# Kernel optimization log

Measured on AMD Instinct MI355X. Metric: run time of the kernel, lower is better.

The kernel has to match this reference:

```python
import jax, jax.numpy as jnp
import numpy as np

V, B, E, T = 100000, 4096, 128, 2
H = 4 * E  # GNN hidden size = 512


def setup_inputs() -> dict:
    key = jax.random.key(0)
    ks = jax.random.split(key, 24)
    stdv = 1.0 / np.sqrt(H)
    u = lambda k, shp: jax.random.uniform(k, shp, jnp.float32, -stdv, stdv)
    return {
        "A": jax.random.uniform(ks[0], (B, 13, 13), jnp.float32),
        "input_ids": jax.random.randint(ks[1], (B, 52), 0, V),
        "emb": jax.random.normal(ks[2], (V, E), jnp.float32) * 0.02,
        "b_ah": u(ks[3], (H,)),
        "w_z": u(ks[4], (H, H)), "b_wz": u(ks[5], (H,)),
        "u_z": u(ks[6], (H, H)), "b_uz": u(ks[7], (H,)),
        "w_r": u(ks[8], (H, H)), "b_wr": u(ks[9], (H,)),
        "u_r": u(ks[10], (H, H)), "b_ur": u(ks[11], (H,)),
        "w": u(ks[12], (H, H)), "b_w": u(ks[13], (H,)),
        "u_": u(ks[14], (H, H)), "b_u": u(ks[15], (H,)),
        "w1": u(ks[16], (H // 2, H)), "b1": u(ks[17], (H // 2,)),
        "w12": u(ks[18], (1, H // 2)), "b12": u(ks[19], (1,)),
        "w2": u(ks[20], (H // 2, H)), "b2": u(ks[21], (H // 2,)),
        "w22": u(ks[22], (1, H // 2)), "b22": u(ks[23], (1,)),
    }


def _sgnn_forward(A, input_ids, emb,
                  b_ah, w_z, b_wz, u_z, b_uz, w_r, b_wr, u_r, b_ur,
                  w, b_w, u_, b_u,
                  w1, b1, w12, b12, w2, b2, w22, b22):
    hid = emb[input_ids]                                        # [B,52,E]
    # cat the 4 fields of each of the 13 nodes -> [B,13,4E]
    h = jnp.concatenate([hid[:, i * 13:(i + 1) * 13, :] for i in range(4)], axis=2)
    At = jnp.swapaxes(A, 1, 2)                                  # [B,13,13]
    for _ in range(T):  # GGNN recurrence, GRU-style cell
        a = jnp.matmul(At, h) + b_ah                            # [B,13,H]
        z = jax.nn.sigmoid(a @ w_z.T + b_wz + h @ u_z.T + b_uz)
        r = jax.nn.sigmoid(a @ w_r.T + b_wr + h @ u_r.T + b_ur)
        c = jnp.tanh(a @ w.T + b_w + (r * h) @ u_.T + b_u)
        h = (1.0 - z) * h + z * c
    gnn_out = h                                                 # [B,13,H]
    ctx = gnn_out[:, 0:8, :]                                    # [B,8,H]
    # repeat(1,5,1).view(5B,8,H): 5 copies of each sample's context
    input_a = jnp.repeat(ctx[:, None, :, :], 5, axis=1).reshape(5 * B, 8, H)
    input_b = gnn_out[:, 8:13, :].reshape(5 * B, H)             # candidates
    # attention over the 8 context events per candidate
    u_a2 = jax.nn.relu(jax.nn.relu(input_a @ w1.T + b1) @ w12.T + b12)  # [5B,8,1]
    u_b2 = jax.nn.relu(jax.nn.relu(input_b @ w2.T + b2) @ w22.T + b22)  # [5B,1]
    u_c = u_a2.reshape(5 * B, 8) + u_b2.reshape(5 * B, 1)
    weight = jnp.exp(jnp.tanh(u_c))
    weight = (weight / jnp.sum(weight, axis=1, keepdims=True))[..., None]
    a_vec = jnp.sum(input_a * weight, axis=1)                   # [5B,H]
    scores = -jnp.sqrt(jnp.sum((a_vec - input_b) ** 2, axis=1))  # euclid metric
    return scores.reshape(B, 5)


def reference(A, input_ids, emb,
              b_ah, w_z, b_wz, u_z, b_uz, w_r, b_wr, u_r, b_ur,
              w, b_w, u_, b_u,
              w1, b1, w12, b12, w2, b2, w22, b22):
    return _sgnn_forward(A, input_ids, emb,
                         b_ah, w_z, b_wz, u_z, b_uz, w_r, b_wr, u_r, b_ur,
                         w, b_w, u_, b_u,
                         w1, b1, w12, b12, w2, b2, w22, b22)
```

## Files before the change

### kernel.cpp

```cpp
#include <hip/hip_runtime.h>
#include <hip/hip_bf16.h>
#include <math.h>

#define HDIM 512

typedef __attribute__((ext_vector_type(8))) __bf16 bf16x8;
typedef __attribute__((ext_vector_type(2))) __bf16 bf16x2;
typedef __attribute__((ext_vector_type(4))) float f32x4;

#define GLOAD16(src, dst) __builtin_amdgcn_global_load_lds( \
    (const __attribute__((address_space(1))) void*)(src),   \
    (__attribute__((address_space(3))) void*)(dst), 16, 0, 0)

__device__ __forceinline__ float sigmoidf_(float x) { return 1.0f / (1.0f + __expf(-x)); }

__global__ __launch_bounds__(256) void f2bf_all(
    const float* __restrict__ w_z, const float* __restrict__ u_z,
    const float* __restrict__ w_r, const float* __restrict__ u_r,
    const float* __restrict__ w_, const float* __restrict__ u_u,
    const float* __restrict__ w1, const float* __restrict__ w2,
    __bf16* __restrict__ Wzb, __bf16* __restrict__ Uzb,
    __bf16* __restrict__ Wrb, __bf16* __restrict__ Urb,
    __bf16* __restrict__ Wb, __bf16* __restrict__ Ub,
    __bf16* __restrict__ W1b, __bf16* __restrict__ W2b) {
    int bid = blockIdx.x;
    const float* s; __bf16* d; int base;
    if (bid < 1024)      { s = w_z; d = Wzb; base = bid; }
    else if (bid < 2048) { s = u_z; d = Uzb; base = bid - 1024; }
    else if (bid < 3072) { s = w_r; d = Wrb; base = bid - 2048; }
    else if (bid < 4096) { s = u_r; d = Urb; base = bid - 3072; }
    else if (bid < 5120) { s = w_;  d = Wb;  base = bid - 4096; }
    else if (bid < 6144) { s = u_u; d = Ub;  base = bid - 5120; }
    else if (bid < 6656) { s = w1;  d = W1b; base = bid - 6144; }
    else                 { s = w2;  d = W2b; base = bid - 6656; }
    int i = base * 256 + threadIdx.x;
    d[i] = (__bf16)s[i];
}

__global__ __launch_bounds__(256) void gather_a(
    const int* __restrict__ ids, const float* __restrict__ emb,
    const float* __restrict__ Ain, const float* __restrict__ bah,
    __bf16* __restrict__ Hbf, __bf16* __restrict__ Abf) {
    int b = blockIdx.x;
    int c2 = threadIdx.x;
    __shared__ float As[169];
    __shared__ int sid[52];
    if (c2 < 169) As[c2] = Ain[b * 169 + c2];
    if (c2 < 52) sid[c2] = ids[b * 52 + c2];
    __syncthreads();
    int c0 = c2 * 2;
    int iseg = c0 >> 7, e = c0 & 127;
    float h0[13], h1[13];
#pragma unroll
    for (int j = 0; j < 13; ++j) {
        int id = sid[iseg * 13 + j];
        float2 hv = *(const float2*)&emb[(size_t)id * 128 + e];
        h0[j] = hv.x;
        h1[j] = hv.y;
        bf16x2 o;
        o[0] = (__bf16)hv.x;
        o[1] = (__bf16)hv.y;
        *(bf16x2*)&Hbf[(size_t)(b * 13 + j) * HDIM + c0] = o;
    }
    float bb0 = bah[c0], bb1 = bah[c0 + 1];
#pragma unroll
    for (int i = 0; i < 13; ++i) {
        float a0 = bb0, a1 = bb1;
#pragma unroll
        for (int j = 0; j < 13; ++j) {
            float a = As[j * 13 + i];
            a0 = fmaf(a, h0[j], a0);
            a1 = fmaf(a, h1[j], a1);
        }
        bf16x2 o;
        o[0] = (__bf16)a0;
        o[1] = (__bf16)a1;
        *(bf16x2*)&Abf[(size_t)(b * 13 + i) * HDIM + c0] = o;
    }
}

__global__ __launch_bounds__(256) void a_kernel(const float* __restrict__ Ain,
                                                const __bf16* __restrict__ Hbf,
                                                const float* __restrict__ bah,
                                                __bf16* __restrict__ Abf) {
    int b = blockIdx.x;
    int c2 = threadIdx.x;
    __shared__ float As[169];
    if (c2 < 169) As[c2] = Ain[b * 169 + c2];
    float h0[13], h1[13];
#pragma unroll
    for (int j = 0; j < 13; ++j) {
        bf16x2 hv = *(const bf16x2*)&Hbf[(size_t)(b * 13 + j) * HDIM + c2 * 2];
        h0[j] = (float)hv[0];
        h1[j] = (float)hv[1];
    }
    __syncthreads();
    float bb0 = bah[c2 * 2], bb1 = bah[c2 * 2 + 1];
#pragma unroll
    for (int i = 0; i < 13; ++i) {
        float acc0 = bb0, acc1 = bb1;
#pragma unroll
        for (int j = 0; j < 13; ++j) {
            float a = As[j * 13 + i];
            acc0 = fmaf(a, h0[j], acc0);
            acc1 = fmaf(a, h1[j], acc1);
        }
        bf16x2 o;
        o[0] = (__bf16)acc0;
        o[1] = (__bf16)acc1;
        *(bf16x2*)&Abf[(size_t)(b * 13 + i) * HDIM + c2 * 2] = o;
    }
}

__global__ __launch_bounds__(512) void zr_fused(
    const __bf16* __restrict__ Abf, const __bf16* __restrict__ Hbf,
    const __bf16* __restrict__ Wz, const __bf16* __restrict__ Uz,
    const __bf16* __restrict__ Wr, const __bf16* __restrict__ Ur,
    const float* __restrict__ bwz, const float* __restrict__ buz,
    const float* __restrict__ bwr, const float* __restrict__ bur,
    __bf16* __restrict__ Zbf, __bf16* __restrict__ RHbf) {
    __shared__ __bf16 lA[2][4096];
    __shared__ __bf16 lB[2][8192];
    int t = threadIdx.x;
    int w = t >> 6, lane = t & 63;
    int role = w & 1;
    int wq = w >> 1;
    int wr2 = wq >> 1, wc2 = wq & 1;
    int m_base = blockIdx.x * 128;
    int n_base = blockIdx.y * 128;

    f32x4 acc[4][4];
#pragma unroll
    for (int i = 0; i < 4; ++i)
#pragma unroll
        for (int j = 0; j < 4; ++j)
#pragma unroll
            for (int q = 0; q < 4; ++q) acc[i][j][q] = 0.0f;

    int srow = t >> 2;
    int scol = ((t & 3) ^ ((t >> 3) & 3)) << 3;
    size_t aoff = (size_t)(m_base + srow) * HDIM + scol;
    size_t boff = (size_t)(n_base + srow) * HDIM + scol;
    int frow = lane & 15, kg = lane >> 4;
    int rsl = kg ^ ((frow >> 1) & 3);

    auto stage = [&](int step, int buf) {
        int seg = step >> 4;
        int kc = (step & 15) << 5;
        const __bf16* Xp = seg ? Hbf : Abf;
        const __bf16* B0 = seg ? Uz : Wz;
        const __bf16* B1 = seg ? Ur : Wr;
        GLOAD16(Xp + aoff + kc, &lA[buf][w * 512]);
        GLOAD16(B0 + boff + kc, &lB[buf][w * 512]);
        GLOAD16(B1 + boff + kc, &lB[buf][4096 + w * 512]);
    };

    stage(0, 0);
    int cur = 0;
    for (int step = 0; step < 32; ++step) {
        if (step < 31) {
            stage(step + 1, cur ^ 1);
            asm volatile("s_waitcnt vmcnt(3)" ::: "memory");
        } else {
            asm volatile("s_waitcnt vmcnt(0)" ::: "memory");
        }
        __builtin_amdgcn_s_barrier();
        bf16x8 af[4], bfr[4];
#pragma unroll
        for (int i = 0; i < 4; ++i) {
            af[i] = *(const bf16x8*)&lA[cur][(wr2 * 64 + i * 16 + frow) * 32 + rsl * 8];
            bfr[i] = *(const bf16x8*)&lB[cur][role * 4096 + (wc2 * 64 + i * 16 + frow) * 32 + rsl * 8];
        }
        __builtin_amdgcn_s_setprio(1);
#pragma unroll
        for (int i = 0; i < 4; ++i)
#pragma unroll
            for (int j = 0; j < 4; ++j)
                acc[i][j] = __builtin_amdgcn_mfma_f32_16x16x32_bf16(af[i], bfr[j], acc[i][j], 0, 0, 0);
        __builtin_amdgcn_s_setprio(0);
        __builtin_amdgcn_s_barrier();
        cur ^= 1;
    }

    int frow4 = (lane >> 4) * 4;
    int fcol = lane & 15;
#pragma unroll
    for (int i = 0; i < 4; ++i) {
#pragma unroll
        for (int j = 0; j < 4; ++j) {
            int col = n_base + wc2 * 64 + j * 16 + fcol;
            float bias = role ? (bwr[col] + bur[col]) : (bwz[col] + buz[col]);
            int rbase = m_base + wr2 * 64 + i * 16 + frow4;
#pragma unroll
            for (int q = 0; q < 4; ++q) {
                size_t off = (size_t)(rbase + q) * HDIM + col;
                float v = sigmoidf_(acc[i][j][q] + bias);
                if (role) {
                    RHbf[off] = (__bf16)(v * (float)Hbf[off]);
                } else {
                    Zbf[off] = (__bf16)v;
                }
            }
        }
    }
}

__global__ __launch_bounds__(512) void c_fused(
    const __bf16* __restrict__ Abf, const __bf16* __restrict__ RHbf,
    const __bf16* __restrict__ W, const __bf16* __restrict__ U,
    const float* __restrict__ bw, const float* __restrict__ bu,
    const __bf16* __restrict__ Zbf, float* __restrict__ Hf, __bf16* __restrict__ Hbf,
    int lastIter) {
    __shared__ __bf16 lA[2][4096];
    __shared__ __bf16 lB[2][4096];
    int t = threadIdx.x;
    int w = t >> 6, lane = t & 63;
    int wr = w >> 2, wc = w & 3;
    int m_base = blockIdx.x * 128;
    int n_base = blockIdx.y * 128;

    f32x4 acc[4][2];
#pragma unroll
    for (int i = 0; i < 4; ++i)
#pragma unroll
        for (int j = 0; j < 2; ++j)
#pragma unroll
            for (int q = 0; q < 4; ++q) acc[i][j][q] = 0.0f;

    int srow = t >> 2;
    int scol = ((t & 3) ^ ((t >> 3) & 3)) << 3;
    size_t aoff = (size_t)(m_base + srow) * HDIM + scol;
    size_t boff = (size_t)(n_base + srow) * HDIM + scol;
    int frow = lane & 15, kg = lane >> 4;
    int rsl = kg ^ ((frow >> 1) & 3);

    auto stage = [&](int step, int buf) {
        int seg = step >> 4;
        int kc = (step & 15) << 5;
        const __bf16* Xp = seg ? RHbf : Abf;
        const __bf16* Wp = seg ? U : W;
        GLOAD16(Xp + aoff + kc, &lA[buf][w * 512]);
        GLOAD16(Wp + boff + kc, &lB[buf][w * 512]);
    };

    stage(0, 0);
    int cur = 0;
    for (int step = 0; step < 32; ++step) {
        if (step < 31) {
            stage(step + 1, cur ^ 1);
            asm volatile("s_waitcnt vmcnt(2)" ::: "memory");
        } else {
            asm volatile("s_waitcnt vmcnt(0)" ::: "memory");
        }
        __builtin_amdgcn_s_barrier();
        bf16x8 af[4], bfr[2];
#pragma unroll
        for (int i = 0; i < 4; ++i)
            af[i] = *(const bf16x8*)&lA[cur][(wr * 64 + i * 16 + frow) * 32 + rsl * 8];
#pragma unroll
        for (int j = 0; j < 2; ++j)
            bfr[j] = *(const bf16x8*)&lB[cur][(wc * 32 + j * 16 + frow) * 32 + rsl * 8];
        __builtin_amdgcn_s_setprio(1);
#pragma unroll
        for (int i = 0; i < 4; ++i)
#pragma unroll
            for (int j = 0; j < 2; ++j)
                acc[i][j] = __builtin_amdgcn_mfma_f32_16x16x32_bf16(af[i], bfr[j], acc[i][j], 0, 0, 0);
        __builtin_amdgcn_s_setprio(0);
        __builtin_amdgcn_s_barrier();
        cur ^= 1;
    }

    int frow4 = (lane >> 4) * 4;
    int fcol = lane & 15;
#pragma unroll
    for (int i = 0; i < 4; ++i) {
#pragma unroll
        for (int j = 0; j < 2; ++j) {
            int col = n_base + wc * 32 + j * 16 + fcol;
            float bias = bw[col] + bu[col];
            int rbase = m_base + wr * 64 + i * 16 + frow4;
#pragma unroll
            for (int q = 0; q < 4; ++q) {
                size_t off = (size_t)(rbase + q) * HDIM + col;
                float v = acc[i][j][q] + bias;
                float x = v > 15.0f ? 15.0f : (v < -15.0f ? -15.0f : v);
                float e = __expf(2.0f * x);
                float cv = (e - 1.0f) / (e + 1.0f);
                float h = (float)Hbf[off];
                float z = (float)Zbf[off];
                float hn = (1.0f - z) * h + z * cv;
                Hbf[off] = (__bf16)hn;
                if (lastIter) Hf[off] = hn;
            }
        }
    }
}

__global__ __launch_bounds__(512) void score_mfma(
    const __bf16* __restrict__ Hbf,
    const __bf16* __restrict__ W1b, const __bf16* __restrict__ W2b,
    const float* __restrict__ b1A, const float* __restrict__ b1B,
    const float* __restrict__ wsA, const float* __restrict__ wsB,
    const float* __restrict__ b2A, const float* __restrict__ b2B,
    float* __restrict__ UA, float* __restrict__ UB, int nblkA) {
    __shared__ __bf16 lA[2][4096];
    __shared__ __bf16 lB[2][8192];
    __shared__ float red[128][5];
    int t = threadIdx.x;
    int w = t >> 6, lane = t & 63;
    int wr = w >> 2, wc = w & 3;

    const __bf16* Wb;
    const float* bias1;
    const float* wsm;
    const float* bias2;
    float* outv;
    int inner, off, m_base;
    if ((int)blockIdx.x < nblkA) {
        Wb = W1b; bias1 = b1A; wsm = wsA; bias2 = b2A; outv = UA;
        inner = 8; off = 0; m_base = blockIdx.x * 128;
    } else {
        Wb = W2b; bias1 = b1B; wsm = wsB; bias2 = b2B; outv = UB;
        inner = 5; off = 8; m_base = (blockIdx.x - nblkA) * 128;
    }

    f32x4 acc[4][4];
#pragma unroll
    for (int i = 0; i < 4; ++i)
#pragma unroll
        for (int j = 0; j < 4; ++j)
#pragma unroll
            for (int q = 0; q < 4; ++q) acc[i][j][q] = 0.0f;

    int srow = t >> 2;
    int scol = ((t & 3) ^ ((t >> 3) & 3)) << 3;
    int mrow = m_base + srow;
    int hrow = (mrow / inner) * 13 + off + (mrow % inner);
    size_t aoff = (size_t)hrow * HDIM + scol;
    size_t boff = (size_t)srow * HDIM + scol;
    int frow = lane & 15, kg = lane >> 4;
    int rsl = kg ^ ((frow >> 1) & 3);

    auto stage = [&](int step, int buf) {
        int kc = step << 5;
        GLOAD16(Hbf + aoff + kc, &lA[buf][w * 512]);
        GLOAD16(Wb + boff + kc, &lB[buf][w * 512]);
        GLOAD16(Wb + boff + (size_t)128 * HDIM + kc, &lB[buf][4096 + w * 512]);
    };

    stage(0, 0);
    int cur = 0;
    for (int step = 0; step < 16; ++step) {
        if (step < 15) {
            stage(step + 1, cur ^ 1);
            asm volatile("s_waitcnt vmcnt(3)" ::: "memory");
        } else {
            asm volatile("s_waitcnt vmcnt(0)" ::: "memory");
        }
        __builtin_amdgcn_s_barrier();
        bf16x8 af[4], bfr[4];
#pragma unroll
        for (int i = 0; i < 4; ++i) {
            af[i] = *(const bf16x8*)&lA[cur][(wr * 64 + i * 16 + frow) * 32 + rsl * 8];
            bfr[i] = *(const bf16x8*)&lB[cur][(wc * 64 + i * 16 + frow) * 32 + rsl * 8];
        }
        __builtin_amdgcn_s_setprio(1);
#pragma unroll
        for (int i = 0; i < 4; ++i)
#pragma unroll
            for (int j = 0; j < 4; ++j)
                acc[i][j] = __builtin_amdgcn_mfma_f32_16x16x32_bf16(af[i], bfr[j], acc[i][j], 0, 0, 0);
        __builtin_amdgcn_s_setprio(0);
        __builtin_amdgcn_s_barrier();
        cur ^= 1;
    }

    int frow4 = (lane >> 4) * 4;
    int fcol = lane & 15;
#pragma unroll
    for (int i = 0; i < 4; ++i) {
#pragma unroll
        for (int q = 0; q < 4; ++q) {
            float s = 0.0f;
#pragma unroll
            for (int j = 0; j < 4; ++j) {
                int col = wc * 64 + j * 16 + fcol;
                float v = acc[i][j][q] + bias1[col];
                v = v > 0.0f ? v : 0.0f;
                s = fmaf(v, wsm[col], s);
            }
            s += __shfl_xor(s, 1);
            s += __shfl_xor(s, 2);
            s += __shfl_xor(s, 4);
            s += __shfl_xor(s, 8);
            if (fcol == 0) red[wr * 64 + i * 16 + frow4 + q][wc] = s;
        }
    }
    __syncthreads();
    if (t < 128) {
        float s = red[t][0] + red[t][1] + red[t][2] + red[t][3] + bias2[0];
        outv[m_base + t] = s > 0.0f ? s : 0.0f;
    }
}

__global__ __launch_bounds__(256) void final_kernel(const float* __restrict__ H,
                                                    const float* __restrict__ UAv,
                                                    const float* __restrict__ UBv,
                                                    float* __restrict__ outv) {
    int b = blockIdx.x;
    int t = threadIdx.x;
    __shared__ float ctx[8][512];
    __shared__ float uas[8], ubs[5];
    __shared__ float red[4];
#pragma unroll
    for (int q = 0; q < 16; ++q) {
        int idx = q * 256 + t;
        int j = idx >> 9, c = idx & 511;
        ctx[j][c] = H[(size_t)(b * 13 + j) * HDIM + c];
    }
    if (t < 8) uas[t] = UAv[b * 8 + t];
    if (t < 5) ubs[t] = UBv[b * 5 + t];
    __syncthreads();
    int c0 = t, c1 = t + 256;
    int wid = t >> 6, lane = t & 63;
    for (int s = 0; s < 5; ++s) {
        float wn[8];
        float sum = 0.0f;
#pragma unroll
        for (int j = 0; j < 8; ++j) {
            wn[j] = __expf(tanhf(uas[j] + ubs[s]));
            sum += wn[j];
        }
        float inv = 1.0f / sum;
        float av0 = 0.0f, av1 = 0.0f;
#pragma unroll
        for (int j = 0; j < 8; ++j) {
            av0 = fmaf(wn[j], ctx[j][c0], av0);
            av1 = fmaf(wn[j], ctx[j][c1], av1);
        }
        av0 *= inv;
        av1 *= inv;
        float d0 = av0 - H[(size_t)(b * 13 + 8 + s) * HDIM + c0];
        float d1 = av1 - H[(size_t)(b * 13 + 8 + s) * HDIM + c1];
        float v = d0 * d0 + d1 * d1;
#pragma unroll
        for (int o = 32; o > 0; o >>= 1) v += __shfl_down(v, o);
        if (lane == 0) red[wid] = v;
        __syncthreads();
        if (t == 0) outv[b * 5 + s] = -sqrtf(red[0] + red[1] + red[2] + red[3]);
        __syncthreads();
    }
}

extern "C" void kernel_launch(void* const* d_in, const int* in_sizes, int n_in,
                              void* d_out, int out_size, void* d_ws, size_t ws_size,
                              hipStream_t stream) {
    const float* Ain  = (const float*)d_in[0];
    const int*   ids  = (const int*)d_in[1];
    const float* emb  = (const float*)d_in[2];
    const float* b_ah = (const float*)d_in[3];
    const float* w_z  = (const float*)d_in[4];
    const float* b_wz = (const float*)d_in[5];
    const float* u_z  = (const float*)d_in[6];
    const float* b_uz = (const float*)d_in[7];
    const float* w_r  = (const float*)d_in[8];
    const float* b_wr = (const float*)d_in[9];
    const float* u_r  = (const float*)d_in[10];
    const float* b_ur = (const float*)d_in[11];
    const float* w_   = (const float*)d_in[12];
    const float* b_w  = (const float*)d_in[13];
    const float* u_u  = (const float*)d_in[14];
    const float* b_u  = (const float*)d_in[15];
    const float* w1   = (const float*)d_in[16];
    const float* b1   = (const float*)d_in[17];
    const float* w12  = (const float*)d_in[18];
    const float* b12  = (const float*)d_in[19];
    const float* w2   = (const float*)d_in[20];
    const float* b2   = (const float*)d_in[21];
    const float* w22  = (const float*)d_in[22];
    const float* b22  = (const float*)d_in[23];
    float* out = (float*)d_out;

    int C = 128;
    {
        const int cands[6] = {4096, 2048, 1024, 512, 256, 128};
        for (int ci = 0; ci < 6; ++ci) {
            int cc = cands[ci];
            size_t rows = (size_t)13 * cc;
            size_t need = rows * 512 * 12
                        + 6 * (size_t)262144 * 2
                        + 2 * (size_t)131072 * 2
                        + (size_t)13 * cc * 4
                        + (4u << 20);
            if (need <= ws_size) { C = cc; break; }
        }
    }
    const int rows = 13 * C;

    char* base = (char*)d_ws;
    __bf16* Wzb = (__bf16*)base; base += 262144 * 2;
    __bf16* Uzb = (__bf16*)base; base += 262144 * 2;
    __bf16* Wrb = (__bf16*)base; base += 262144 * 2;
    __bf16* Urb = (__bf16*)base; base += 262144 * 2;
    __bf16* Wb  = (__bf16*)base; base += 262144 * 2;
    __bf16* Ub  = (__bf16*)base; base += 262144 * 2;
    __bf16* W1b = (__bf16*)base; base += 131072 * 2;
    __bf16* W2b = (__bf16*)base; base += 131072 * 2;
    float* UA  = (float*)base; base += (size_t)8 * C * 4;
    float* UB  = (float*)base; base += (size_t)5 * C * 4;
    float* Hf  = (float*)base; base += (size_t)rows * 512 * 4;
    __bf16* Hbf  = (__bf16*)base; base += (size_t)rows * 512 * 2;
    __bf16* Abf  = (__bf16*)base; base += (size_t)rows * 512 * 2;
    __bf16* RHbf = (__bf16*)base; base += (size_t)rows * 512 * 2;
    __bf16* Zbf  = (__bf16*)base; base += (size_t)rows * 512 * 2;

    f2bf_all<<<7168, 256, 0, stream>>>(w_z, u_z, w_r, u_r, w_, u_u, w1, w2,
                                       Wzb, Uzb, Wrb, Urb, Wb, Ub, W1b, W2b);

    dim3 ggrid(rows / 128, 4);
    int nblkA = 8 * C / 128;
    int nblkB = 5 * C / 128;
    for (int g0 = 0; g0 < 4096; g0 += C) {
        gather_a<<<C, 256, 0, stream>>>(ids + (size_t)g0 * 52, emb,
                                        Ain + (size_t)g0 * 169, b_ah, Hbf, Abf);
        zr_fused<<<ggrid, 512, 0, stream>>>(Abf, Hbf, Wzb, Uzb, Wrb, Urb,
                                            b_wz, b_uz, b_wr, b_ur, Zbf, RHbf);
        c_fused<<<ggrid, 512, 0, stream>>>(Abf, RHbf, Wb, Ub, b_w, b_u, Zbf, Hf, Hbf, 0);
        a_kernel<<<C, 256, 0, stream>>>(Ain + (size_t)g0 * 169, Hbf, b_ah, Abf);
        zr_fused<<<ggrid, 512, 0, stream>>>(Abf, Hbf, Wzb, Uzb, Wrb, Urb,
                                            b_wz, b_uz, b_wr, b_ur, Zbf, RHbf);
        c_fused<<<ggrid, 512, 0, stream>>>(Abf, RHbf, Wb, Ub, b_w, b_u, Zbf, Hf, Hbf, 1);

        score_mfma<<<nblkA + nblkB, 512, 0, stream>>>(Hbf, W1b, W2b, b1, b2, w12, w22,
                                                      b12, b22, UA, UB, nblkA);
        final_kernel<<<C, 256, 0, stream>>>(Hf, UA, UB, out + (size_t)g0 * 5);
    }
}
```

Measured before the change: 809.1 us.

## Split c_fused K-loop across two warp groups with LDS reduction

The c_fused GEMM now splits its 1024-long K dimension between two halves of the workgroup: four waves handle the A·W segment and four handle the RH·U segment, both running concurrently with 64x64 per-wave tiles. Each step stages both segments into 64KB of LDS, which halves the number of pipeline steps and barriers. The second half writes its partial accumulators to LDS and the first half adds them in the epilogue. The cost is more registers per wave, larger LDS use that may lower occupancy, and an extra LDS reduction pass.

```diff
diff --git a/kernel.cpp b/kernel.cpp
--- a/kernel.cpp
+++ b/kernel.cpp
@@ -211,87 +211,107 @@
     const float* __restrict__ bw, const float* __restrict__ bu,
     const __bf16* __restrict__ Zbf, float* __restrict__ Hf, __bf16* __restrict__ Hbf,
     int lastIter) {
-    __shared__ __bf16 lA[2][4096];
-    __shared__ __bf16 lB[2][4096];
+    __shared__ __attribute__((aligned(16))) char smem[65536];
+    __bf16* lA0 = (__bf16*)smem;
+    __bf16* lB0 = (__bf16*)(smem + 16384);
+    __bf16* lA1 = (__bf16*)(smem + 32768);
+    __bf16* lB1 = (__bf16*)(smem + 49152);
+    float* comb = (float*)smem;
+
     int t = threadIdx.x;
     int w = t >> 6, lane = t & 63;
-    int wr = w >> 2, wc = w & 3;
+    int kh = w >> 2;
+    int q = w & 3;
+    int wr = q >> 1, wc = q & 1;
     int m_base = blockIdx.x * 128;
     int n_base = blockIdx.y * 128;
 
-    f32x4 acc[4][2];
+    f32x4 acc[4][4];
 #pragma unroll
     for (int i = 0; i < 4; ++i)
 #pragma unroll
-        for (int j = 0; j < 2; ++j)
-#pragma unroll
-            for (int q = 0; q < 4; ++q) acc[i][j][q] = 0.0f;
+        for (int j = 0; j < 4; ++j)
+#pragma unroll
+            for (int p = 0; p < 4; ++p) acc[i][j][p] = 0.0f;
 
     int srow = t >> 2;
     int scol = ((t & 3) ^ ((t >> 3) & 3)) << 3;
-    size_t aoff = (size_t)(m_base + srow) * HDIM + scol;
-    size_t boff = (size_t)(n_base + srow) * HDIM + scol;
+    size_t moff = (size_t)(m_base + srow) * HDIM + scol;
+    size_t noff = (size_t)(n_base + srow) * HDIM + scol;
     int frow = lane & 15, kg = lane >> 4;
     int rsl = kg ^ ((frow >> 1) & 3);
 
     auto stage = [&](int step, int buf) {
-        int seg = step >> 4;
-        int kc = (step & 15) << 5;
-        const __bf16* Xp = seg ? RHbf : Abf;
-        const __bf16* Wp = seg ? U : W;
-        GLOAD16(Xp + aoff + kc, &lA[buf][w * 512]);
-        GLOAD16(Wp + boff + kc, &lB[buf][w * 512]);
+        int kc = step << 5;
+        GLOAD16(Abf + moff + kc, lA0 + buf * 4096 + w * 512);
+        GLOAD16(W + noff + kc, lB0 + buf * 4096 + w * 512);
+        GLOAD16(RHbf + moff + kc, lA1 + buf * 4096 + w * 512);
+        GLOAD16(U + noff + kc, lB1 + buf * 4096 + w * 512);
     };
+
+    const __bf16* mySrcA = kh ? lA1 : lA0;
+    const __bf16* mySrcB = kh ? lB1 : lB0;
 
     stage(0, 0);
     int cur = 0;
-    for (int step = 0; step < 32; ++step) {
-        if (step < 31) {
+    for (int step = 0; step < 16; ++step) {
+        if (step < 15) {
             stage(step + 1, cur ^ 1);
-            asm volatile("s_waitcnt vmcnt(2)" ::: "memory");
+            asm volatile("s_waitcnt vmcnt(4)" ::: "memory");
         } else {
             asm volatile("s_waitcnt vmcnt(0)" ::: "memory");
         }
         __builtin_amdgcn_s_barrier();
-        bf16x8 af[4], bfr[2];
+        bf16x8 af[4], bfr[4];
+#pragma unroll
+        for (int i = 0; i < 4; ++i) {
+            af[i] = *(const bf16x8*)&mySrcA[cur * 4096 + (wr * 64 + i * 16 + frow) * 32 + rsl * 8];
+            bfr[i] = *(const bf16x8*)&mySrcB[cur * 4096 + (wc * 64 + i * 16 + frow) * 32 + rsl * 8];
+        }
+        __builtin_amdgcn_s_setprio(1);
 #pragma unroll
         for (int i = 0; i < 4; ++i)
-            af[i] = *(const bf16x8*)&lA[cur][(wr * 64 + i * 16 + frow) * 32 + rsl * 8];
-#pragma unroll
-        for (int j = 0; j < 2; ++j)
-            bfr[j] = *(const bf16x8*)&lB[cur][(wc * 32 + j * 16 + frow) * 32 + rsl * 8];
-        __builtin_amdgcn_s_setprio(1);
-#pragma unroll
-        for (int i = 0; i < 4; ++i)
-#pragma unroll
-            for (int j = 0; j < 2; ++j)
+#pragma unroll
+            for (int j = 0; j < 4; ++j)
                 acc[i][j] = __builtin_amdgcn_mfma_f32_16x16x32_bf16(af[i], bfr[j], acc[i][j], 0, 0, 0);
         __builtin_amdgcn_s_setprio(0);
         __builtin_amdgcn_s_barrier();
         cur ^= 1;
     }
 
-    int frow4 = (lane >> 4) * 4;
-    int fcol = lane & 15;
-#pragma unroll
-    for (int i = 0; i < 4; ++i) {
-#pragma unroll
-        for (int j = 0; j < 2; ++j) {
-            int col = n_base + wc * 32 + j * 16 + fcol;
-            float bias = bw[col] + bu[col];
-            int rbase = m_base + wr * 64 + i * 16 + frow4;
-#pragma unroll
-            for (int q = 0; q < 4; ++q) {
-                size_t off = (size_t)(rbase + q) * HDIM + col;
-                float v = acc[i][j][q] + bias;
-                float x = v > 15.0f ? 15.0f : (v < -15.0f ? -15.0f : v);
-                float e = __expf(2.0f * x);
-                float cv = (e - 1.0f) / (e + 1.0f);
-                float h = (float)Hbf[off];
-                float z = (float)Zbf[off];
-                float hn = (1.0f - z) * h + z * cv;
-                Hbf[off] = (__bf16)hn;
-                if (lastIter) Hf[off] = hn;
+    __syncthreads();
+    if (kh == 1) {
+#pragma unroll
+        for (int i = 0; i < 4; ++i)
+#pragma unroll
+            for (int j = 0; j < 4; ++j)
+                *(f32x4*)&comb[q * 4096 + (i * 4 + j) * 256 + lane * 4] = acc[i][j];
+    }
+    __syncthreads();
+    if (kh == 0) {
+        int frow4 = (lane >> 4) * 4;
+        int fcol = lane & 15;
+#pragma unroll
+        for (int i = 0; i < 4; ++i) {
+#pragma unroll
+            for (int j = 0; j < 4; ++j) {
+                f32x4 part = *(const f32x4*)&comb[q * 4096 + (i * 4 + j) * 256 + lane * 4];
+                int col = n_base + wc * 64 + j * 16 + fcol;
+                float bias = bw[col] + bu[col];
+                int rbase = m_base + wr * 64 + i * 16 + frow4;
+#pragma unroll
+                for (int p = 0; p < 4; ++p) {
+                    size_t off = (size_t)(rbase + p) * HDIM + col;
+                    float v = acc[i][j][p] + part[p] + bias;
+                    float x = v > 15.0f ? 15.0f : (v < -15.0f ? -15.0f : v);
+                    float e = __expf(2.0f * x);
+                    float cv = (e - 1.0f) / (e + 1.0f);
+                    float h = (float)Hbf[off];
+                    float z = (float)Zbf[off];
+                    float hn = (1.0f - z) * h + z * cv;
+                    Hbf[off] = (__bf16)hn;
+                    if (lastIter) Hf[off] = hn;
+                }
             }
         }
     }
```

Measured after the change: 828.4 us. 2.4% more time.
